# Kernel tuning notes

Measured on AMD Instinct MI355X. Metric: run time of the kernel, lower is better.

Reference implementation:

```python
import jax, jax.numpy as jnp
import numpy as np

EPS = 1e-8  # torch F.cosine_similarity default eps

N, M, PLANES = 4096, 4096, 512


def setup_inputs() -> dict:
    key = jax.random.key(0)
    k1, k2, k3, k4 = jax.random.split(key, 4)
    pre = jax.random.normal(k1, (N, PLANES), dtype=jnp.float32)
    cur = jax.random.normal(k2, (M, PLANES), dtype=jnp.float32)
    adj = jax.random.uniform(k3, (N, M), dtype=jnp.float32)
    stdv = 1.0 / np.sqrt(PLANES)
    weight = jax.random.uniform(k4, (PLANES, PLANES), dtype=jnp.float32,
                                minval=-stdv, maxval=stdv)
    return {"pre": pre, "cur": cur, "adj": adj, "weight": weight}


def reference(pre, cur, adj, weight):
    # --- GraphConvolution ---
    pre_w = pre @ weight            # [N, P]
    cur_w = cur @ weight            # [M, P]
    pre_h = adj @ cur_w             # [N, P]  adj_norm @ cur_
    cur_h = adj.T @ pre_w           # [M, P]  adj_t_norm @ pre_

    # --- edge_update: tan(cosine_similarity) for all (i, j) pairs, fused ---
    # cosine_similarity(x, y) = (x . y) / (max(||x||, eps) * max(||y||, eps))
    pre_norm = jnp.maximum(jnp.linalg.norm(pre_h, axis=1, keepdims=True), EPS)
    cur_norm = jnp.maximum(jnp.linalg.norm(cur_h, axis=1, keepdims=True), EPS)
    pre_n = pre_h / pre_norm        # [N, P]
    cur_n = cur_h / cur_norm        # [M, P]
    cos = pre_n @ cur_n.T           # [N, M]
    adj_out = jnp.tan(cos)          # [N, M]
    score = adj_out.reshape(-1)     # [N*M], row-major == i * M + j ordering
    return (score, adj_out)
```

## Files before the change

kernel.cpp:

```cpp
#include <hip/hip_runtime.h>

typedef unsigned short ushort_t;
typedef __attribute__((ext_vector_type(8))) short short8;
typedef __attribute__((ext_vector_type(4))) float f32x4;

__device__ __forceinline__ ushort_t f2bf(float x) {
  union { float f; unsigned u; } v; v.f = x;
  unsigned r = v.u + 0x7fffu + ((v.u >> 16) & 1u);
  return (ushort_t)(r >> 16);
}
__device__ __forceinline__ float bf2f(ushort_t h) {
  union { unsigned u; float f; } v; v.u = ((unsigned)h) << 16;
  return v.f;
}

__device__ __forceinline__ void async_cp16(const ushort_t* g, ushort_t* lds) {
  __builtin_amdgcn_global_load_lds(
      (const __attribute__((address_space(1))) unsigned int*)g,
      (__attribute__((address_space(3))) unsigned int*)lds, 16, 0, 0);
}

template <int MT, int NT, int BKT, int EPI>
__device__ __forceinline__ void gemm_core(
    const ushort_t* __restrict__ A, int lda,
    const ushort_t* __restrict__ B, int ldb,
    int K,
    ushort_t* sA, ushort_t* sB,
    ushort_t* Cb, float* Cf0, float* Cf1, int ldc,
    const float* __restrict__ ip, const float* __restrict__ ic) {
  constexpr int MI = MT / 32, NI = NT / 32, KU = BKT / 32;
  constexpr int LPR = BKT / 8;
  constexpr int RPC = 256 / LPR;
  const int t = threadIdx.x;
  const int wave = t >> 6, lane = t & 63;
  const int lm = lane & 15, lq = lane >> 4;
  const int wr = wave >> 1, wc = wave & 1;

  f32x4 acc[MI][NI] = {};

  const ushort_t* ga = A + (size_t)(t / LPR) * lda + (t % LPR) * 8;
  const ushort_t* gb = B + (size_t)(t / LPR) * ldb + (t % LPR) * 8;
  ushort_t* sA0 = sA + wave * 512;
  ushort_t* sB0 = sB + wave * 512;

  for (int k0 = 0; k0 < K; k0 += BKT) {
#pragma unroll
    for (int j = 0; j < MT / RPC; j++)
      async_cp16(ga + k0 + (size_t)j * RPC * lda, sA0 + j * 2048);
#pragma unroll
    for (int j = 0; j < NT / RPC; j++)
      async_cp16(gb + k0 + (size_t)j * RPC * ldb, sB0 + j * 2048);
    __syncthreads();

#pragma unroll
    for (int ku = 0; ku < KU; ku++) {
      short8 af[MI], bf4[NI];
#pragma unroll
      for (int i = 0; i < MI; i++)
        af[i] = *(const short8*)(sA + (wr * (MT / 2) + i * 16 + lm) * BKT +
                                 ku * 32 + lq * 8);
#pragma unroll
      for (int i = 0; i < NI; i++)
        bf4[i] = *(const short8*)(sB + (wc * (NT / 2) + i * 16 + lm) * BKT +
                                  ku * 32 + lq * 8);
#pragma unroll
      for (int mt = 0; mt < MI; mt++)
#pragma unroll
        for (int nt = 0; nt < NI; nt++)
          acc[mt][nt] = __builtin_amdgcn_mfma_f32_16x16x32_bf16(
              af[mt], bf4[nt], acc[mt][nt], 0, 0, 0);
    }
    __syncthreads();
  }

#pragma unroll
  for (int mt = 0; mt < MI; mt++) {
    int rb = wr * (MT / 2) + mt * 16 + lq * 4;
#pragma unroll
    for (int nt = 0; nt < NI; nt++) {
      int c = wc * (NT / 2) + nt * 16 + lm;
#pragma unroll
      for (int r = 0; r < 4; r++) {
        size_t idx = (size_t)(rb + r) * ldc + c;
        if (EPI == 1) {
          Cb[idx] = f2bf(acc[mt][nt][r]);
        } else {
          float v = __tanf(acc[mt][nt][r] * ip[rb + r] * ic[c]);
          Cf0[idx] = v;
          Cf1[idx] = v;
        }
      }
    }
  }
}

__global__ __launch_bounds__(256) void convT(
    const float* __restrict__ in, ushort_t* __restrict__ outn,
    ushort_t* __restrict__ outt, int n) {
  __shared__ float tile[64][65];
  const int t = threadIdx.x;
  const int r0 = blockIdx.y * 64, c0 = blockIdx.x * 64;
  const int cr = t >> 4;
  const int cc = (t & 15) * 4;
#pragma unroll
  for (int p = 0; p < 4; p++) {
    int r = cr + p * 16;
    float4 v = *(const float4*)(in + (size_t)(r0 + r) * n + c0 + cc);
    tile[r][cc + 0] = v.x; tile[r][cc + 1] = v.y;
    tile[r][cc + 2] = v.z; tile[r][cc + 3] = v.w;
    ushort4 o;
    o.x = f2bf(v.x); o.y = f2bf(v.y); o.z = f2bf(v.z); o.w = f2bf(v.w);
    *(ushort4*)(outn + (size_t)(r0 + r) * n + c0 + cc) = o;
  }
  __syncthreads();
#pragma unroll
  for (int p = 0; p < 4; p++) {
    int r = cr + p * 16;
    ushort4 o;
    o.x = f2bf(tile[cc + 0][r]); o.y = f2bf(tile[cc + 1][r]);
    o.z = f2bf(tile[cc + 2][r]); o.w = f2bf(tile[cc + 3][r]);
    *(ushort4*)(outt + (size_t)(c0 + r) * n + r0 + cc) = o;
  }
}

__global__ __launch_bounds__(256) void k1_gemm(
    const ushort_t* __restrict__ wt_t, const float* __restrict__ pre,
    const float* __restrict__ cur, ushort_t* __restrict__ pw_t) {
  __shared__ __align__(16) ushort_t sA[64 * 32];
  __shared__ __align__(16) ushort_t sB[128 * 32];
  const int t = threadIdx.x;
  const int wave = t >> 6, lane = t & 63;
  const int lm = lane & 15, lq = lane >> 4;
  const int wr = wave >> 1, wc = wave & 1;
  const int bm = blockIdx.x & 7, bn = blockIdx.x >> 3;
  const int n0 = bn * 128;
  const ushort_t* A = wt_t + (size_t)bm * 64 * 512;
  const float* Bf = (n0 < 4096) ? (pre + (size_t)n0 * 512)
                                : (cur + (size_t)(n0 - 4096) * 512);
  ushort_t* C = pw_t + (size_t)bm * 64 * 8192 + n0;

  f32x4 acc[2][4] = {};
  const ushort_t* ga = A + (size_t)(t >> 2) * 512 + (t & 3) * 8;
  const float* gb = Bf + (size_t)(t >> 2) * 512 + (t & 3) * 8;
  ushort_t* sA0 = sA + wave * 512;
  ushort_t* sBw = sB + t * 8;

  for (int k0 = 0; k0 < 512; k0 += 32) {
    async_cp16(ga + k0, sA0);
    float4 u0 = *(const float4*)(gb + k0);
    float4 u1 = *(const float4*)(gb + k0 + 4);
    float4 u2 = *(const float4*)(gb + k0 + (size_t)64 * 512);
    float4 u3 = *(const float4*)(gb + k0 + (size_t)64 * 512 + 4);
    short8 w0, w1;
    w0[0] = (short)f2bf(u0.x); w0[1] = (short)f2bf(u0.y);
    w0[2] = (short)f2bf(u0.z); w0[3] = (short)f2bf(u0.w);
    w0[4] = (short)f2bf(u1.x); w0[5] = (short)f2bf(u1.y);
    w0[6] = (short)f2bf(u1.z); w0[7] = (short)f2bf(u1.w);
    w1[0] = (short)f2bf(u2.x); w1[1] = (short)f2bf(u2.y);
    w1[2] = (short)f2bf(u2.z); w1[3] = (short)f2bf(u2.w);
    w1[4] = (short)f2bf(u3.x); w1[5] = (short)f2bf(u3.y);
    w1[6] = (short)f2bf(u3.z); w1[7] = (short)f2bf(u3.w);
    *(short8*)(sBw) = w0;
    *(short8*)(sBw + 2048) = w1;
    __syncthreads();

    short8 af[2], bf4[4];
#pragma unroll
    for (int i = 0; i < 2; i++)
      af[i] = *(const short8*)(sA + (wr * 32 + i * 16 + lm) * 32 + lq * 8);
#pragma unroll
    for (int i = 0; i < 4; i++)
      bf4[i] = *(const short8*)(sB + (wc * 64 + i * 16 + lm) * 32 + lq * 8);
#pragma unroll
    for (int mt = 0; mt < 2; mt++)
#pragma unroll
      for (int nt = 0; nt < 4; nt++)
        acc[mt][nt] = __builtin_amdgcn_mfma_f32_16x16x32_bf16(
            af[mt], bf4[nt], acc[mt][nt], 0, 0, 0);
    __syncthreads();
  }

#pragma unroll
  for (int mt = 0; mt < 2; mt++) {
    int rb = wr * 32 + mt * 16 + lq * 4;
#pragma unroll
    for (int nt = 0; nt < 4; nt++) {
      int c = wc * 64 + nt * 16 + lm;
#pragma unroll
      for (int r = 0; r < 4; r++)
        C[(size_t)(rb + r) * 8192 + c] = f2bf(acc[mt][nt][r]);
    }
  }
}

__global__ __launch_bounds__(256) void k2_gemm(
    const ushort_t* __restrict__ adj, const ushort_t* __restrict__ adj_t,
    const ushort_t* __restrict__ pw_t, ushort_t* __restrict__ pn) {
  __shared__ __align__(16) ushort_t sA[128 * 64];
  __shared__ __align__(16) ushort_t sB[64 * 64];
  const int b = blockIdx.x;
  const int half = b >> 8, bb = b & 255;
  const int bn = (bb >> 3) & 7;
  const int bm = (bb & 7) | ((bb >> 6) << 3);
  const ushort_t* A = (half ? adj_t : adj) + (size_t)bm * 128 * 4096;
  const ushort_t* B = pw_t + (size_t)bn * 64 * 8192 + (half ? 0 : 4096);
  ushort_t* C = pn + (half ? (size_t)4096 * 512 : 0) +
                (size_t)bm * 128 * 512 + bn * 64;
  gemm_core<128, 64, 64, 1>(A, 4096, B, 8192, 4096, sA, sB, C, nullptr,
                            nullptr, 512, nullptr, nullptr);
}

__global__ __launch_bounds__(256) void invnorm_kernel(
    const ushort_t* __restrict__ pn, float* __restrict__ invn) {
  const int t = threadIdx.x;
  const int wave = t >> 6, lane = t & 63;
  const size_t row = (size_t)blockIdx.x * 4 + wave;
  const ushort_t* p = pn + row * 512 + lane * 8;
  short8 v = *(const short8*)p;
  float s = 0.f;
#pragma unroll
  for (int i = 0; i < 8; i++) {
    float f = bf2f((ushort_t)v[i]);
    s += f * f;
  }
#pragma unroll
  for (int off = 32; off > 0; off >>= 1) s += __shfl_xor(s, off, 64);
  if (lane == 0) invn[row] = 1.0f / fmaxf(sqrtf(s), 1e-8f);
}

__global__ __launch_bounds__(256) void k3_gemm(
    const ushort_t* __restrict__ pn, const float* __restrict__ invn,
    float* __restrict__ out) {
  __shared__ __align__(16) ushort_t sA[128 * 32];
  __shared__ __align__(16) ushort_t sB[128 * 32];
  const int bm = blockIdx.x & 31, bn = blockIdx.x >> 5;
  const ushort_t* A = pn + (size_t)bm * 128 * 512;
  const ushort_t* B = pn + (size_t)4096 * 512 + (size_t)bn * 128 * 512;
  float* C0 = out + (size_t)bm * 128 * 4096 + bn * 128;
  gemm_core<128, 128, 32, 2>(A, 512, B, 512, 512, sA, sB, nullptr, C0,
                             C0 + (size_t)4096 * 4096, 4096,
                             invn + bm * 128, invn + 4096 + bn * 128);
}

extern "C" void kernel_launch(void* const* d_in, const int* in_sizes, int n_in,
                              void* d_out, int out_size, void* d_ws,
                              size_t ws_size, hipStream_t stream) {
  const float* pre = (const float*)d_in[0];
  const float* cur = (const float*)d_in[1];
  const float* adj = (const float*)d_in[2];
  const float* wt  = (const float*)d_in[3];
  float* out = (float*)d_out;

  ushort_t* adj_bf = (ushort_t*)d_ws;
  ushort_t* adj_t  = adj_bf + (size_t)4096 * 4096;
  ushort_t* pw_t   = adj_t + (size_t)4096 * 4096;
  ushort_t* pn     = pw_t + (size_t)512 * 8192;
  ushort_t* wt_t   = pn + (size_t)8192 * 512;
  ushort_t* wt_bf  = wt_t + (size_t)512 * 512;
  float*    invn   = (float*)(wt_bf + (size_t)512 * 512);

  convT<<<dim3(64, 64), 256, 0, stream>>>(adj, adj_bf, adj_t, 4096);
  convT<<<dim3(8, 8), 256, 0, stream>>>(wt, wt_bf, wt_t, 512);
  k1_gemm<<<512, 256, 0, stream>>>(wt_t, pre, cur, pw_t);
  k2_gemm<<<512, 256, 0, stream>>>(adj_bf, adj_t, pw_t, pn);
  invnorm_kernel<<<2048, 256, 0, stream>>>(pn, invn);
  k3_gemm<<<1024, 256, 0, stream>>>(pn, invn, out);
}
```

Before: 332.7 us.

## Pre-convert inputs to bf16, reuse shared gemm core, and enlarge K tiles

```diff
diff --git a/kernel.cpp b/kernel.cpp
--- a/kernel.cpp
+++ b/kernel.cpp
@@ -123,81 +123,40 @@
   }
 }
 
+__global__ __launch_bounds__(256) void xcvt(
+    const float* __restrict__ pre, const float* __restrict__ cur,
+    ushort_t* __restrict__ xbf) {
+  const size_t i = ((size_t)blockIdx.x * 256 + threadIdx.x) * 8;
+  const float* src =
+      (i < (size_t)4096 * 512) ? (pre + i) : (cur + (i - (size_t)4096 * 512));
+  float4 a = *(const float4*)(src);
+  float4 b = *(const float4*)(src + 4);
+  short8 o;
+  o[0] = (short)f2bf(a.x); o[1] = (short)f2bf(a.y);
+  o[2] = (short)f2bf(a.z); o[3] = (short)f2bf(a.w);
+  o[4] = (short)f2bf(b.x); o[5] = (short)f2bf(b.y);
+  o[6] = (short)f2bf(b.z); o[7] = (short)f2bf(b.w);
+  *(short8*)(xbf + i) = o;
+}
+
 __global__ __launch_bounds__(256) void k1_gemm(
-    const ushort_t* __restrict__ wt_t, const float* __restrict__ pre,
-    const float* __restrict__ cur, ushort_t* __restrict__ pw_t) {
-  __shared__ __align__(16) ushort_t sA[64 * 32];
-  __shared__ __align__(16) ushort_t sB[128 * 32];
-  const int t = threadIdx.x;
-  const int wave = t >> 6, lane = t & 63;
-  const int lm = lane & 15, lq = lane >> 4;
-  const int wr = wave >> 1, wc = wave & 1;
+    const ushort_t* __restrict__ wt_t, const ushort_t* __restrict__ xbf,
+    ushort_t* __restrict__ pw_t) {
+  __shared__ __align__(16) ushort_t sA[64 * 64];
+  __shared__ __align__(16) ushort_t sB[128 * 64];
   const int bm = blockIdx.x & 7, bn = blockIdx.x >> 3;
-  const int n0 = bn * 128;
   const ushort_t* A = wt_t + (size_t)bm * 64 * 512;
-  const float* Bf = (n0 < 4096) ? (pre + (size_t)n0 * 512)
-                                : (cur + (size_t)(n0 - 4096) * 512);
-  ushort_t* C = pw_t + (size_t)bm * 64 * 8192 + n0;
-
-  f32x4 acc[2][4] = {};
-  const ushort_t* ga = A + (size_t)(t >> 2) * 512 + (t & 3) * 8;
-  const float* gb = Bf + (size_t)(t >> 2) * 512 + (t & 3) * 8;
-  ushort_t* sA0 = sA + wave * 512;
-  ushort_t* sBw = sB + t * 8;
-
-  for (int k0 = 0; k0 < 512; k0 += 32) {
-    async_cp16(ga + k0, sA0);
-    float4 u0 = *(const float4*)(gb + k0);
-    float4 u1 = *(const float4*)(gb + k0 + 4);
-    float4 u2 = *(const float4*)(gb + k0 + (size_t)64 * 512);
-    float4 u3 = *(const float4*)(gb + k0 + (size_t)64 * 512 + 4);
-    short8 w0, w1;
-    w0[0] = (short)f2bf(u0.x); w0[1] = (short)f2bf(u0.y);
-    w0[2] = (short)f2bf(u0.z); w0[3] = (short)f2bf(u0.w);
-    w0[4] = (short)f2bf(u1.x); w0[5] = (short)f2bf(u1.y);
-    w0[6] = (short)f2bf(u1.z); w0[7] = (short)f2bf(u1.w);
-    w1[0] = (short)f2bf(u2.x); w1[1] = (short)f2bf(u2.y);
-    w1[2] = (short)f2bf(u2.z); w1[3] = (short)f2bf(u2.w);
-    w1[4] = (short)f2bf(u3.x); w1[5] = (short)f2bf(u3.y);
-    w1[6] = (short)f2bf(u3.z); w1[7] = (short)f2bf(u3.w);
-    *(short8*)(sBw) = w0;
-    *(short8*)(sBw + 2048) = w1;
-    __syncthreads();
-
-    short8 af[2], bf4[4];
-#pragma unroll
-    for (int i = 0; i < 2; i++)
-      af[i] = *(const short8*)(sA + (wr * 32 + i * 16 + lm) * 32 + lq * 8);
-#pragma unroll
-    for (int i = 0; i < 4; i++)
-      bf4[i] = *(const short8*)(sB + (wc * 64 + i * 16 + lm) * 32 + lq * 8);
-#pragma unroll
-    for (int mt = 0; mt < 2; mt++)
-#pragma unroll
-      for (int nt = 0; nt < 4; nt++)
-        acc[mt][nt] = __builtin_amdgcn_mfma_f32_16x16x32_bf16(
-            af[mt], bf4[nt], acc[mt][nt], 0, 0, 0);
-    __syncthreads();
-  }
-
-#pragma unroll
-  for (int mt = 0; mt < 2; mt++) {
-    int rb = wr * 32 + mt * 16 + lq * 4;
-#pragma unroll
-    for (int nt = 0; nt < 4; nt++) {
-      int c = wc * 64 + nt * 16 + lm;
-#pragma unroll
-      for (int r = 0; r < 4; r++)
-        C[(size_t)(rb + r) * 8192 + c] = f2bf(acc[mt][nt][r]);
-    }
-  }
+  const ushort_t* B = xbf + (size_t)bn * 128 * 512;
+  ushort_t* C = pw_t + (size_t)bm * 64 * 8192 + bn * 128;
+  gemm_core<64, 128, 64, 1>(A, 512, B, 512, 512, sA, sB, C, nullptr, nullptr,
+                            8192, nullptr, nullptr);
 }
 
 __global__ __launch_bounds__(256) void k2_gemm(
     const ushort_t* __restrict__ adj, const ushort_t* __restrict__ adj_t,
     const ushort_t* __restrict__ pw_t, ushort_t* __restrict__ pn) {
-  __shared__ __align__(16) ushort_t sA[128 * 64];
-  __shared__ __align__(16) ushort_t sB[64 * 64];
+  __shared__ __align__(16) ushort_t sA[128 * 128];
+  __shared__ __align__(16) ushort_t sB[64 * 128];
   const int b = blockIdx.x;
   const int half = b >> 8, bb = b & 255;
   const int bn = (bb >> 3) & 7;
@@ -206,8 +165,8 @@
   const ushort_t* B = pw_t + (size_t)bn * 64 * 8192 + (half ? 0 : 4096);
   ushort_t* C = pn + (half ? (size_t)4096 * 512 : 0) +
                 (size_t)bm * 128 * 512 + bn * 64;
-  gemm_core<128, 64, 64, 1>(A, 4096, B, 8192, 4096, sA, sB, C, nullptr,
-                            nullptr, 512, nullptr, nullptr);
+  gemm_core<128, 64, 128, 1>(A, 4096, B, 8192, 4096, sA, sB, C, nullptr,
+                             nullptr, 512, nullptr, nullptr);
 }
 
 __global__ __launch_bounds__(256) void invnorm_kernel(
@@ -231,13 +190,13 @@
 __global__ __launch_bounds__(256) void k3_gemm(
     const ushort_t* __restrict__ pn, const float* __restrict__ invn,
     float* __restrict__ out) {
-  __shared__ __align__(16) ushort_t sA[128 * 32];
-  __shared__ __align__(16) ushort_t sB[128 * 32];
+  __shared__ __align__(16) ushort_t sA[128 * 64];
+  __shared__ __align__(16) ushort_t sB[128 * 64];
   const int bm = blockIdx.x & 31, bn = blockIdx.x >> 5;
   const ushort_t* A = pn + (size_t)bm * 128 * 512;
   const ushort_t* B = pn + (size_t)4096 * 512 + (size_t)bn * 128 * 512;
   float* C0 = out + (size_t)bm * 128 * 4096 + bn * 128;
-  gemm_core<128, 128, 32, 2>(A, 512, B, 512, 512, sA, sB, nullptr, C0,
+  gemm_core<128, 128, 64, 2>(A, 512, B, 512, 512, sA, sB, nullptr, C0,
                              C0 + (size_t)4096 * 4096, 4096,
                              invn + bm * 128, invn + 4096 + bn * 128);
 }
@@ -258,10 +217,12 @@
   ushort_t* wt_t   = pn + (size_t)8192 * 512;
   ushort_t* wt_bf  = wt_t + (size_t)512 * 512;
   float*    invn   = (float*)(wt_bf + (size_t)512 * 512);
+  ushort_t* xbf    = (ushort_t*)(invn + 8192);
 
   convT<<<dim3(64, 64), 256, 0, stream>>>(adj, adj_bf, adj_t, 4096);
   convT<<<dim3(8, 8), 256, 0, stream>>>(wt, wt_bf, wt_t, 512);
-  k1_gemm<<<512, 256, 0, stream>>>(wt_t, pre, cur, pw_t);
+  xcvt<<<2048, 256, 0, stream>>>(pre, cur, xbf);
+  k1_gemm<<<512, 256, 0, stream>>>(wt_t, xbf, pw_t);
   k2_gemm<<<512, 256, 0, stream>>>(adj_bf, adj_t, pw_t, pn);
   invnorm_kernel<<<2048, 256, 0, stream>>>(pn, invn);
   k3_gemm<<<1024, 256, 0, stream>>>(pn, invn, out);
```

Result: slower. 360.0 us (+8.2%).
